# Kernel tuning notes

Measured on AMD Instinct MI355X. Metric: run time of the kernel, lower is better.

## Reference

```python
import jax, jax.numpy as jnp
import numpy as np

DIM = 1024
HEADS = 16
HEAD_DIM = DIM // HEADS
RPE_K = 16
B, T = 4, 1024


def setup_inputs() -> dict:
    key = jax.random.key(0)
    ks = jax.random.split(key, 12)
    s = 1.0 / np.sqrt(DIM)
    inp = {
        'q': jax.random.normal(ks[0], (B, T, DIM), jnp.float32),
        'k': jax.random.normal(ks[1], (B, T, DIM), jnp.float32),
        'v': jax.random.normal(ks[2], (B, T, DIM), jnp.float32),
        'Wq': jax.random.normal(ks[3], (DIM, DIM), jnp.float32) * s,
        'bq': jnp.zeros((DIM,), jnp.float32),
        'Wk': jax.random.normal(ks[4], (DIM, DIM), jnp.float32) * s,
        'bk': jnp.zeros((DIM,), jnp.float32),
        'Wv': jax.random.normal(ks[5], (DIM, DIM), jnp.float32) * s,
        'bv': jnp.zeros((DIM,), jnp.float32),
        'rpe_w': jax.random.normal(ks[6], (2 * RPE_K + 1, 2 * HEAD_DIM), jnp.float32) * 0.02,
        'Wo': jax.random.normal(ks[7], (DIM, DIM), jnp.float32) * s,
        'bo': jnp.zeros((DIM,), jnp.float32),
    }
    return inp


def reference(q, k, v, Wq, bq, Wk, bk, Wv, bv, rpe_w, Wo, bo):
    b, ql = q.shape[:2]
    kl = k.shape[1]
    split = lambda x: x.reshape(b, -1, HEADS, HEAD_DIM).transpose(0, 2, 1, 3)  # b h t d
    qh = split(q @ Wq.T + bq)
    kh = split(k @ Wk.T + bk)
    vh = split(v @ Wv.T + bv)
    # note: original scales q BEFORE both the k-dot and the rpe_q einsum
    qh = qh / np.sqrt(HEAD_DIM)
    # relative distance table (constant ints)
    idx = jnp.arange(max(ql, kl))
    dist = jnp.clip(idx[:, None] - idx[None, :], -RPE_K, RPE_K) + RPE_K
    dist = dist[:ql, :kl]
    rpe = rpe_w[dist]                      # (ql, kl, 2*HEAD_DIM)
    rpe_q, rpe_v = jnp.split(rpe, 2, axis=-1)
    energy = jnp.einsum('bhqd,bhkd->bhqk', qh, kh)
    energy = energy + jnp.einsum('bhqd,qkd->bhqk', qh, rpe_q)
    alignment = jax.nn.softmax(energy, axis=-1)
    context = jnp.einsum('bhqk,bhkd->bhqd', alignment, vh)
    context = context + jnp.einsum('bhqk,qkd->bhqd', alignment, rpe_v)
    context = context.transpose(0, 2, 1, 3).reshape(b, ql, DIM)
    out = context @ Wo.T + bo
    return (out, alignment)
```

## Files before the change

kernel.cpp:

```cpp
#include <hip/hip_runtime.h>
#include <stdint.h>

typedef unsigned short u16;
typedef unsigned int   u32;
typedef short bf16x8 __attribute__((ext_vector_type(8)));
typedef float floatx4 __attribute__((ext_vector_type(4)));

#define OFF_XQ   0u
#define OFF_XK   4194304u
#define OFF_XV   8388608u
#define OFF_WQ   12582912u
#define OFF_WK   13631488u
#define OFF_WV   14680064u
#define OFF_WO   15728640u
#define OFF_QH   16777216u
#define OFF_KH   20971520u
#define OFF_VT   25165824u
#define OFF_CTX  29360128u

__device__ __forceinline__ u16 f2b(float f){
  u32 u = __float_as_uint(f);
  u = (u + 0x7fffu + ((u >> 16) & 1u)) >> 16;
  return (u16)u;
}
__device__ __forceinline__ float b2f(u16 h){
  return __uint_as_float(((u32)h) << 16);
}

__global__ __launch_bounds__(256) void convert_kernel(
    const float* __restrict__ q, const float* __restrict__ k, const float* __restrict__ v,
    const float* __restrict__ Wq, const float* __restrict__ Wk, const float* __restrict__ Wv,
    const float* __restrict__ Wo, u16* __restrict__ ws){
  int y = blockIdx.y;
  const float* src; u16* dst; int n;
  switch(y){
    case 0: src=q;  dst=ws+OFF_XQ; n=4194304; break;
    case 1: src=k;  dst=ws+OFF_XK; n=4194304; break;
    case 2: src=v;  dst=ws+OFF_XV; n=4194304; break;
    case 3: src=Wq; dst=ws+OFF_WQ; n=1048576; break;
    case 4: src=Wk; dst=ws+OFF_WK; n=1048576; break;
    case 5: src=Wv; dst=ws+OFF_WV; n=1048576; break;
    default:src=Wo; dst=ws+OFF_WO; n=1048576; break;
  }
  int idx = (blockIdx.x*256 + threadIdx.x)*4;
  if (idx >= n) return;
  float4 f = *(const float4*)(src + idx);
  ushort4 o;
  o.x = f2b(f.x); o.y = f2b(f.y); o.z = f2b(f.z); o.w = f2b(f.w);
  *(ushort4*)(dst + idx) = o;
}

template<int MODE>
__global__ __launch_bounds__(256) void gemm_kernel(
    const u16* __restrict__ A0, const u16* __restrict__ B0,
    const float* __restrict__ b0, const float* __restrict__ b1, const float* __restrict__ b2,
    u16* __restrict__ ws, float* __restrict__ outF){
  constexpr int BN = (MODE==1) ? 64 : 128;
  constexpr int NJ = BN/32;
  __shared__ u16 As[128][32];
  __shared__ u16 Bs[BN][32];
  int z = (MODE==0) ? blockIdx.z : 0;
  const u16* A  = A0 + (size_t)z*4194304u;
  const u16* Bm = B0 + (size_t)z*1048576u;
  const float* bias = (MODE==0) ? (z==0?b0:(z==1?b1:b2)) : b0;
  int tid  = threadIdx.x;
  int lane = tid & 63, wave = tid >> 6;
  int wm = (wave>>1)*64, wn = (wave&1)*(BN/2);
  int m_base = blockIdx.y*128, n_base = blockIdx.x*BN;
  floatx4 acc[4][NJ] = {};
  int fr = lane & 15, fo = (lane>>4)*8;
  int srow = lane >> 2, sseg = (lane & 3)*8;
  u16* AsW0 = &As[wave*32][0];
  u16* AsW1 = &As[wave*32+16][0];
  const u16* Ag0 = A  + (size_t)(m_base + wave*32      + srow)*1024 + sseg;
  const u16* Ag1 = A  + (size_t)(m_base + wave*32 + 16 + srow)*1024 + sseg;
  u16* BsW0; u16* BsW1; const u16* Bg0; const u16* Bg1;
  if constexpr (BN==128){
    BsW0 = &Bs[wave*32][0];    BsW1 = &Bs[wave*32+16][0];
    Bg0 = Bm + (size_t)(n_base + wave*32      + srow)*1024 + sseg;
    Bg1 = Bm + (size_t)(n_base + wave*32 + 16 + srow)*1024 + sseg;
  } else {
    BsW0 = &Bs[wave*16][0];    BsW1 = nullptr;
    Bg0 = Bm + (size_t)(n_base + wave*16 + srow)*1024 + sseg;
    Bg1 = nullptr;
  }
  for (int kb = 0; kb < 1024; kb += 32){
    __builtin_amdgcn_global_load_lds((const u32*)(Ag0 + kb), (u32*)AsW0, 16, 0, 0);
    __builtin_amdgcn_global_load_lds((const u32*)(Ag1 + kb), (u32*)AsW1, 16, 0, 0);
    __builtin_amdgcn_global_load_lds((const u32*)(Bg0 + kb), (u32*)BsW0, 16, 0, 0);
    if constexpr (BN==128)
      __builtin_amdgcn_global_load_lds((const u32*)(Bg1 + kb), (u32*)BsW1, 16, 0, 0);
    __syncthreads();
    bf16x8 af[4], bfr[NJ];
    #pragma unroll
    for (int i=0;i<4;i++)
      af[i]  = *(const bf16x8*)(&As[wm + i*16 + fr][fo]);
    #pragma unroll
    for (int j=0;j<NJ;j++)
      bfr[j] = *(const bf16x8*)(&Bs[wn + j*16 + fr][fo]);
    #pragma unroll
    for (int i=0;i<4;i++)
      #pragma unroll
      for (int j=0;j<NJ;j++)
        acc[i][j] = __builtin_amdgcn_mfma_f32_16x16x32_bf16(af[i], bfr[j], acc[i][j], 0,0,0);
    __syncthreads();
  }
  int col = lane & 15, rb = (lane>>4)*4;
  #pragma unroll
  for (int i=0;i<4;i++){
    #pragma unroll
    for (int j=0;j<NJ;j++){
      int nn = n_base + wn + j*16 + col;
      float bv = bias[nn];
      #pragma unroll
      for (int r=0;r<4;r++){
        int mm = m_base + wm + i*16 + rb + r;
        float v = acc[i][j][r] + bv;
        if (MODE==0){
          if (z==0) v *= 0.125f;
          int b = mm>>10, t = mm&1023, h = nn>>6, d = nn&63;
          u32 base = (z==0)?OFF_QH:((z==1)?OFF_KH:OFF_VT);
          u32 idx = ((u32)(b*16+h))<<16;
          idx += (z==2) ? ((u32)(d<<10)+(u32)t) : ((u32)(t<<6)+(u32)d);
          ws[base + idx] = f2b(v);
        } else {
          outF[(size_t)mm*1024 + nn] = v;
        }
      }
    }
  }
}

__global__ __launch_bounds__(256) void attn_kernel(
    const u16* __restrict__ ws, const float* __restrict__ rpe_w,
    float* __restrict__ d_out, u16* __restrict__ ctx){
  __shared__ u16   qs[16][64];
  __shared__ float proj[16][33];
  __shared__ float ssum[4][16][4];
  __shared__ float slds[16][33];
  __shared__ float linv16[16];
  __shared__ float oacc[4][16][64];

  int bid = blockIdx.x;
  int qt = bid & 63, bh = bid >> 6;
  int q0 = qt * 16;
  int tid = threadIdx.x, lane = tid & 63, wave = tid >> 6;
  int col = lane & 15, g = lane >> 4, rb = g*4, fo = g*8;

  const u16* qh = ws + OFF_QH + (size_t)bh*65536;
  const u16* kh = ws + OFF_KH + (size_t)bh*65536;
  const u16* vT = ws + OFF_VT + (size_t)bh*65536;

  if (tid < 128){
    int r = tid >> 3, c = (tid & 7)*8;
    *(uint4*)(&qs[r][c]) = *(const uint4*)(qh + (size_t)(q0+r)*64 + c);
  }
  for (int i = tid; i < 16*33; i += 256) ((float*)slds)[i] = 0.f;
  __syncthreads();

  for (int i = tid; i < 16*33; i += 256){
    int r = i / 33, t = i - r*33;
    float s = 0.f;
    #pragma unroll
    for (int d=0; d<64; d++) s += b2f(qs[r][d]) * rpe_w[t*128 + d];
    proj[r][t] = s;
  }
  __syncthreads();

  bf16x8 bq0 = *(const bf16x8*)(&qs[col][fo]);
  bf16x8 bq1 = *(const bf16x8*)(&qs[col][32 + fo]);
  int qg = q0 + col;
  int kw = wave*256;

  float tot = 0.f, lo = 0.f, hi = 0.f;
  for (int sp = 0; sp < 8; ++sp){
    int kbase = kw + sp*32;
    #pragma unroll
    for (int t=0; t<2; ++t){
      const u16* kp = kh + (size_t)(kbase + 16*t + col)*64 + fo;
      bf16x8 ak0 = *(const bf16x8*)(kp);
      bf16x8 ak1 = *(const bf16x8*)(kp + 32);
      floatx4 s4 = {0.f,0.f,0.f,0.f};
      s4 = __builtin_amdgcn_mfma_f32_16x16x32_bf16(ak0, bq0, s4, 0,0,0);
      s4 = __builtin_amdgcn_mfma_f32_16x16x32_bf16(ak1, bq1, s4, 0,0,0);
      #pragma unroll
      for (int r=0;r<4;r++){
        int key = kbase + 16*t + rb + r, dd = qg - key;
        int bkt = min(max(dd, -16), 16) + 16;
        float p = __expf(s4[r] + proj[col][bkt]);
        tot += p;
        if      (key <= qg - 16) lo += p;
        else if (key >= qg + 16) hi += p;
      }
    }
  }
  tot += __shfl_xor(tot,16); tot += __shfl_xor(tot,32);
  lo  += __shfl_xor(lo, 16); lo  += __shfl_xor(lo, 32);
  hi  += __shfl_xor(hi, 16); hi  += __shfl_xor(hi, 32);
  if (lane < 16){
    ssum[wave][lane][0] = tot; ssum[wave][lane][1] = lo; ssum[wave][lane][2] = hi;
  }
  __syncthreads();
  if (tid < 16){
    float T = ssum[0][tid][0]+ssum[1][tid][0]+ssum[2][tid][0]+ssum[3][tid][0];
    float L = ssum[0][tid][1]+ssum[1][tid][1]+ssum[2][tid][1]+ssum[3][tid][1];
    float H = ssum[0][tid][2]+ssum[1][tid][2]+ssum[2][tid][2]+ssum[3][tid][2];
    float li = 1.f / T;
    linv16[tid] = li;
    slds[tid][32] = L*li;
    slds[tid][0]  = H*li;
  }
  __syncthreads();
  float li_c = linv16[col];

  floatx4 o4[4] = {};
  float* outA = d_out + 4194304u + ((size_t)(bh*1024 + q0))*1024;
  for (int sp = 0; sp < 8; ++sp){
    int kbase = kw + sp*32;
    float p0[4], p1[4];
    {
      const u16* kp = kh + (size_t)(kbase + col)*64 + fo;
      bf16x8 ak0 = *(const bf16x8*)(kp);
      bf16x8 ak1 = *(const bf16x8*)(kp + 32);
      floatx4 s4 = {0.f,0.f,0.f,0.f};
      s4 = __builtin_amdgcn_mfma_f32_16x16x32_bf16(ak0, bq0, s4, 0,0,0);
      s4 = __builtin_amdgcn_mfma_f32_16x16x32_bf16(ak1, bq1, s4, 0,0,0);
      #pragma unroll
      for (int r=0;r<4;r++){
        int key = kbase + rb + r, dd = qg - key;
        int bkt = min(max(dd, -16), 16) + 16;
        float p = __expf(s4[r] + proj[col][bkt]) * li_c;
        p0[r] = p;
        if (dd > -16 && dd < 16) slds[col][dd+16] = p;
      }
    }
    {
      const u16* kp = kh + (size_t)(kbase + 16 + col)*64 + fo;
      bf16x8 ak0 = *(const bf16x8*)(kp);
      bf16x8 ak1 = *(const bf16x8*)(kp + 32);
      floatx4 s4 = {0.f,0.f,0.f,0.f};
      s4 = __builtin_amdgcn_mfma_f32_16x16x32_bf16(ak0, bq0, s4, 0,0,0);
      s4 = __builtin_amdgcn_mfma_f32_16x16x32_bf16(ak1, bq1, s4, 0,0,0);
      #pragma unroll
      for (int r=0;r<4;r++){
        int key = kbase + 16 + rb + r, dd = qg - key;
        int bkt = min(max(dd, -16), 16) + 16;
        float p = __expf(s4[r] + proj[col][bkt]) * li_c;
        p1[r] = p;
        if (dd > -16 && dd < 16) slds[col][dd+16] = p;
      }
    }
    float pa[8];
    #pragma unroll
    for (int j=0;j<8;++j){
      int gs = ((g<<1)&3) + (j>>2);
      int src = col + (gs<<4);
      float a = __shfl(p0[j&3], src);
      float b = __shfl(p1[j&3], src);
      pa[j] = (g & 2) ? b : a;
    }
    {
      float* wp = outA + (size_t)col*1024 + kbase + 8*g;
      float4 w0 = {pa[0],pa[1],pa[2],pa[3]};
      float4 w1 = {pa[4],pa[5],pa[6],pa[7]};
      *(float4*)wp = w0; *(float4*)(wp+4) = w1;
    }
    bf16x8 af;
    #pragma unroll
    for (int j=0;j<8;++j) af[j] = (short)f2b(pa[j]);
    #pragma unroll
    for (int dt=0; dt<4; ++dt){
      bf16x8 bv = *(const bf16x8*)(vT + (size_t)(dt*16 + col)*1024 + kbase + fo);
      o4[dt] = __builtin_amdgcn_mfma_f32_16x16x32_bf16(af, bv, o4[dt], 0,0,0);
    }
  }
  #pragma unroll
  for (int dt=0; dt<4; ++dt)
    #pragma unroll
    for (int r=0;r<4;++r)
      oacc[wave][rb+r][dt*16 + col] = o4[dt][r];
  __syncthreads();

  {
    int b = bh >> 4, h = bh & 15, d2 = wave*16 + col;
    #pragma unroll
    for (int r=0;r<4;++r){
      int row = rb + r;
      float ov = oacc[0][row][d2] + oacc[1][row][d2] + oacc[2][row][d2] + oacc[3][row][d2];
      float sv = 0.f;
      #pragma unroll
      for (int t=0;t<33;++t) sv += slds[row][t] * rpe_w[t*128 + 64 + d2];
      ctx[((size_t)(b*1024 + q0 + row))*1024 + h*64 + d2] = f2b(ov + sv);
    }
  }
}

extern "C" void kernel_launch(void* const* d_in, const int* in_sizes, int n_in,
                              void* d_out, int out_size, void* d_ws, size_t ws_size,
                              hipStream_t stream){
  const float* q  = (const float*)d_in[0];
  const float* k  = (const float*)d_in[1];
  const float* v  = (const float*)d_in[2];
  const float* Wq = (const float*)d_in[3];
  const float* bq = (const float*)d_in[4];
  const float* Wk = (const float*)d_in[5];
  const float* bk = (const float*)d_in[6];
  const float* Wv = (const float*)d_in[7];
  const float* bv = (const float*)d_in[8];
  const float* rpe= (const float*)d_in[9];
  const float* Wo = (const float*)d_in[10];
  const float* bo = (const float*)d_in[11];
  u16* ws = (u16*)d_ws;
  float* out = (float*)d_out;

  convert_kernel<<<dim3(4096,7), 256, 0, stream>>>(q,k,v,Wq,Wk,Wv,Wo, ws);
  gemm_kernel<0><<<dim3(8,32,3), 256, 0, stream>>>(ws+OFF_XQ, ws+OFF_WQ, bq, bk, bv, ws, nullptr);
  attn_kernel<<<dim3(4096), 256, 0, stream>>>(ws, rpe, out, ws+OFF_CTX);
  gemm_kernel<1><<<dim3(16,32), 256, 0, stream>>>(ws+OFF_CTX, ws+OFF_WO, bo, nullptr, nullptr, ws, out);
}
```

Before: 639.3 us.

## Cache softmax exponentials in registers to avoid recomputing QK scores in second pass

The attention kernel now keeps the 64 exponentiated scores per lane in registers after the first pass, so the second pass no longer reloads K or recomputes QK MFMAs and exps. It feeds the unnormalized probabilities straight into 16x16x16 bf16 MFMAs through inline asm, which avoids the cross-lane shuffles. Normalization is deferred to the final context write. Alignment output is transposed through a padded LDS scratch buffer that also holds the reduction. The cost is much higher register pressure (p4[16] floatx4), which risks lower occupancy, plus hand-inserted s_nop hazards around the asm MFMAs.

```diff
diff --git a/kernel.cpp b/kernel.cpp
--- a/kernel.cpp
+++ b/kernel.cpp
@@ -4,6 +4,7 @@
 typedef unsigned short u16;
 typedef unsigned int   u32;
 typedef short bf16x8 __attribute__((ext_vector_type(8)));
+typedef short bf16x4 __attribute__((ext_vector_type(4)));
 typedef float floatx4 __attribute__((ext_vector_type(4)));
 
 #define OFF_XQ   0u
@@ -139,7 +140,7 @@
   __shared__ float ssum[4][16][4];
   __shared__ float slds[16][33];
   __shared__ float linv16[16];
-  __shared__ float oacc[4][16][64];
+  __shared__ float upool[4224];
 
   int bid = blockIdx.x;
   int qt = bid & 63, bh = bid >> 6;
@@ -171,27 +172,35 @@
   bf16x8 bq1 = *(const bf16x8*)(&qs[col][32 + fo]);
   int qg = q0 + col;
   int kw = wave*256;
-
+  float pj_hi = proj[col][0];
+  float pj_lo = proj[col][32];
+
+  floatx4 p4[16];
   float tot = 0.f, lo = 0.f, hi = 0.f;
-  for (int sp = 0; sp < 8; ++sp){
-    int kbase = kw + sp*32;
-    #pragma unroll
-    for (int t=0; t<2; ++t){
-      const u16* kp = kh + (size_t)(kbase + 16*t + col)*64 + fo;
-      bf16x8 ak0 = *(const bf16x8*)(kp);
-      bf16x8 ak1 = *(const bf16x8*)(kp + 32);
-      floatx4 s4 = {0.f,0.f,0.f,0.f};
-      s4 = __builtin_amdgcn_mfma_f32_16x16x32_bf16(ak0, bq0, s4, 0,0,0);
-      s4 = __builtin_amdgcn_mfma_f32_16x16x32_bf16(ak1, bq1, s4, 0,0,0);
-      #pragma unroll
-      for (int r=0;r<4;r++){
-        int key = kbase + 16*t + rb + r, dd = qg - key;
-        int bkt = min(max(dd, -16), 16) + 16;
-        float p = __expf(s4[r] + proj[col][bkt]);
-        tot += p;
-        if      (key <= qg - 16) lo += p;
-        else if (key >= qg + 16) hi += p;
-      }
+  const u16* khw = kh + (size_t)(kw + col)*64 + fo;
+  #pragma unroll
+  for (int it = 0; it < 16; ++it){
+    const u16* kp = khw + it*1024;
+    bf16x8 ak0 = *(const bf16x8*)(kp);
+    bf16x8 ak1 = *(const bf16x8*)(kp + 32);
+    floatx4 s4 = {0.f,0.f,0.f,0.f};
+    s4 = __builtin_amdgcn_mfma_f32_16x16x32_bf16(ak0, bq0, s4, 0,0,0);
+    s4 = __builtin_amdgcn_mfma_f32_16x16x32_bf16(ak1, bq1, s4, 0,0,0);
+    #pragma unroll
+    for (int r=0;r<4;r++){
+      int key = kw + it*16 + rb + r;
+      int dd = qg - key;
+      float pjv;
+      bool mid = false;
+      if      (dd >= 16)  pjv = pj_lo;
+      else if (dd <= -16) pjv = pj_hi;
+      else { pjv = proj[col][dd+16]; mid = true; }
+      float p = __expf(s4[r] + pjv);
+      p4[it][r] = p;
+      tot += p;
+      if (mid) slds[col][dd+16] = p;
+      else if (dd >= 16) lo += p;
+      else hi += p;
     }
   }
   tot += __shfl_xor(tot,16); tot += __shfl_xor(tot,32);
@@ -205,80 +214,52 @@
     float T = ssum[0][tid][0]+ssum[1][tid][0]+ssum[2][tid][0]+ssum[3][tid][0];
     float L = ssum[0][tid][1]+ssum[1][tid][1]+ssum[2][tid][1]+ssum[3][tid][1];
     float H = ssum[0][tid][2]+ssum[1][tid][2]+ssum[2][tid][2]+ssum[3][tid][2];
-    float li = 1.f / T;
-    linv16[tid] = li;
-    slds[tid][32] = L*li;
-    slds[tid][0]  = H*li;
+    linv16[tid] = 1.f / T;
+    slds[tid][32] = L;
+    slds[tid][0]  = H;
   }
   __syncthreads();
   float li_c = linv16[col];
 
   floatx4 o4[4] = {};
+  float* Ptw = upool + wave*560;
   float* outA = d_out + 4194304u + ((size_t)(bh*1024 + q0))*1024;
-  for (int sp = 0; sp < 8; ++sp){
-    int kbase = kw + sp*32;
-    float p0[4], p1[4];
-    {
-      const u16* kp = kh + (size_t)(kbase + col)*64 + fo;
-      bf16x8 ak0 = *(const bf16x8*)(kp);
-      bf16x8 ak1 = *(const bf16x8*)(kp + 32);
-      floatx4 s4 = {0.f,0.f,0.f,0.f};
-      s4 = __builtin_amdgcn_mfma_f32_16x16x32_bf16(ak0, bq0, s4, 0,0,0);
-      s4 = __builtin_amdgcn_mfma_f32_16x16x32_bf16(ak1, bq1, s4, 0,0,0);
+  int rq = lane >> 2, cb = (lane & 3)*8;
+  #pragma unroll
+  for (int it = 0; it < 16; ++it){
+    int kbase = kw + it*16;
+    bf16x4 af;
+    af[0] = (short)f2b(p4[it][0]);
+    af[1] = (short)f2b(p4[it][1]);
+    af[2] = (short)f2b(p4[it][2]);
+    af[3] = (short)f2b(p4[it][3]);
+    #pragma unroll
+    for (int dt=0; dt<4; ++dt){
+      bf16x4 bv = *(const bf16x4*)(vT + (size_t)(dt*16 + col)*1024 + kbase + rb);
+      asm("s_nop 1\n\tv_mfma_f32_16x16x16_bf16 %0, %1, %2, %0"
+          : "+v"(o4[dt]) : "v"(af), "v"(bv));
+    }
+    #pragma unroll
+    for (int r=0;r<4;r++)
+      Ptw[col*35 + (it&1)*16 + rb + r] = p4[it][r] * li_c;
+    if (it & 1){
+      const float* prow = Ptw + rq*35 + cb;
+      float4 w0 = {prow[0],prow[1],prow[2],prow[3]};
+      float4 w1 = {prow[4],prow[5],prow[6],prow[7]};
+      float* gp = outA + (size_t)rq*1024 + kw + (it-1)*16 + cb;
+      *(float4*)gp = w0; *(float4*)(gp+4) = w1;
+    }
+  }
+  asm volatile("s_nop 7\n\ts_nop 7");
+  __syncthreads();
+  {
+    float* oa = upool + wave*1056;
+    #pragma unroll
+    for (int dt=0; dt<4; ++dt)
       #pragma unroll
-      for (int r=0;r<4;r++){
-        int key = kbase + rb + r, dd = qg - key;
-        int bkt = min(max(dd, -16), 16) + 16;
-        float p = __expf(s4[r] + proj[col][bkt]) * li_c;
-        p0[r] = p;
-        if (dd > -16 && dd < 16) slds[col][dd+16] = p;
-      }
-    }
-    {
-      const u16* kp = kh + (size_t)(kbase + 16 + col)*64 + fo;
-      bf16x8 ak0 = *(const bf16x8*)(kp);
-      bf16x8 ak1 = *(const bf16x8*)(kp + 32);
-      floatx4 s4 = {0.f,0.f,0.f,0.f};
-      s4 = __builtin_amdgcn_mfma_f32_16x16x32_bf16(ak0, bq0, s4, 0,0,0);
-      s4 = __builtin_amdgcn_mfma_f32_16x16x32_bf16(ak1, bq1, s4, 0,0,0);
-      #pragma unroll
-      for (int r=0;r<4;r++){
-        int key = kbase + 16 + rb + r, dd = qg - key;
-        int bkt = min(max(dd, -16), 16) + 16;
-        float p = __expf(s4[r] + proj[col][bkt]) * li_c;
-        p1[r] = p;
-        if (dd > -16 && dd < 16) slds[col][dd+16] = p;
-      }
-    }
-    float pa[8];
-    #pragma unroll
-    for (int j=0;j<8;++j){
-      int gs = ((g<<1)&3) + (j>>2);
-      int src = col + (gs<<4);
-      float a = __shfl(p0[j&3], src);
-      float b = __shfl(p1[j&3], src);
-      pa[j] = (g & 2) ? b : a;
-    }
-    {
-      float* wp = outA + (size_t)col*1024 + kbase + 8*g;
-      float4 w0 = {pa[0],pa[1],pa[2],pa[3]};
-      float4 w1 = {pa[4],pa[5],pa[6],pa[7]};
-      *(float4*)wp = w0; *(float4*)(wp+4) = w1;
-    }
-    bf16x8 af;
-    #pragma unroll
-    for (int j=0;j<8;++j) af[j] = (short)f2b(pa[j]);
-    #pragma unroll
-    for (int dt=0; dt<4; ++dt){
-      bf16x8 bv = *(const bf16x8*)(vT + (size_t)(dt*16 + col)*1024 + kbase + fo);
-      o4[dt] = __builtin_amdgcn_mfma_f32_16x16x32_bf16(af, bv, o4[dt], 0,0,0);
-    }
-  }
-  #pragma unroll
-  for (int dt=0; dt<4; ++dt)
-    #pragma unroll
-    for (int r=0;r<4;++r)
-      oacc[wave][rb+r][dt*16 + col] = o4[dt][r];
+      for (int r=0;r<4;++r)
+        oa[(rb+r)*66 + dt*16 + col] = o4[dt][r];
+  }
   __syncthreads();
 
   {
@@ -286,11 +267,13 @@
     #pragma unroll
     for (int r=0;r<4;++r){
       int row = rb + r;
-      float ov = oacc[0][row][d2] + oacc[1][row][d2] + oacc[2][row][d2] + oacc[3][row][d2];
+      float ov = upool[row*66 + d2] + upool[1056 + row*66 + d2]
+               + upool[2112 + row*66 + d2] + upool[3168 + row*66 + d2];
       float sv = 0.f;
       #pragma unroll
       for (int t=0;t<33;++t) sv += slds[row][t] * rpe_w[t*128 + 64 + d2];
-      ctx[((size_t)(b*1024 + q0 + row))*1024 + h*64 + d2] = f2b(ov + sv);
+      float li_r = linv16[row];
+      ctx[((size_t)(b*1024 + q0 + row))*1024 + h*64 + d2] = f2b((ov + sv) * li_r);
     }
   }
 }
```

New measurement: 699.8 us. 9.5% more time.
